# Kernel optimization log

Hardware: AMD Instinct MI355X
Metric: run time of the kernel (lower is better)

Reference implementation:

```python
import jax, jax.numpy as jnp
import numpy as np

H = 512; NH = 8; L = 2; NPRED = 26; MAXF = 5; FF = 4 * H


def _ln(x, w, b, eps=1e-5):
    m = x.mean(-1, keepdims=True)
    v = ((x - m) ** 2).mean(-1, keepdims=True)
    return (x - m) / jnp.sqrt(v + eps) * w + b


def _gelu(x):
    return jax.nn.gelu(x, approximate=False)


def _mha(q_in, kv_in, in_w, in_b, out_w, out_b, nh=NH):
    # PyTorch nn.MultiheadAttention math (batch_first), no mask, eval mode.
    h = q_in.shape[-1]; dh = h // nh
    Wq, Wk, Wv = in_w[:h], in_w[h:2 * h], in_w[2 * h:]
    bq, bk, bv = in_b[:h], in_b[h:2 * h], in_b[2 * h:]
    B, Tq, _ = q_in.shape
    Tk = kv_in.shape[1]
    q = (q_in @ Wq.T + bq).reshape(B, Tq, nh, dh)
    k = (kv_in @ Wk.T + bk).reshape(B, Tk, nh, dh)
    v = (kv_in @ Wv.T + bv).reshape(B, Tk, nh, dh)
    s = jnp.einsum('bqhd,bkhd->bhqk', q, k) / jnp.sqrt(jnp.asarray(dh, q.dtype))
    a = jax.nn.softmax(s, axis=-1)
    o = jnp.einsum('bhqk,bkhd->bqhd', a, v).reshape(B, Tq, h)
    return o @ out_w.T + out_b


def setup_inputs():
    key = jax.random.key(0)
    ks = iter(jax.random.split(key, 48))
    r = lambda *s: jax.random.normal(next(ks), s, jnp.float32) * 0.02
    inp = {
        'temporal_context': jax.random.normal(next(ks), (16, 10, H), jnp.float32),
        'object_features': jax.random.normal(next(ks), (16, 20, H), jnp.float32),
        'future_queries': r(MAXF, H),
        'sa_in_w': r(L, 3 * H, H), 'sa_in_b': jnp.zeros((L, 3 * H), jnp.float32),
        'sa_out_w': r(L, H, H), 'sa_out_b': jnp.zeros((L, H), jnp.float32),
        'ca_in_w': r(L, 3 * H, H), 'ca_in_b': jnp.zeros((L, 3 * H), jnp.float32),
        'ca_out_w': r(L, H, H), 'ca_out_b': jnp.zeros((L, H), jnp.float32),
        'ff1_w': r(L, FF, H), 'ff1_b': jnp.zeros((L, FF), jnp.float32),
        'ff2_w': r(L, H, FF), 'ff2_b': jnp.zeros((L, H), jnp.float32),
        'n1_w': jnp.ones((L, H), jnp.float32), 'n1_b': jnp.zeros((L, H), jnp.float32),
        'n2_w': jnp.ones((L, H), jnp.float32), 'n2_b': jnp.zeros((L, H), jnp.float32),
        'n3_w': jnp.ones((L, H), jnp.float32), 'n3_b': jnp.zeros((L, H), jnp.float32),
        'norm_w': jnp.ones((H,), jnp.float32), 'norm_b': jnp.zeros((H,), jnp.float32),
        'pe1_w': r(H, 3 * H), 'pe1_b': jnp.zeros((H,), jnp.float32),
        'pe2_w': r(H, H), 'pe2_b': jnp.zeros((H,), jnp.float32),
        'pred_w': r(NPRED, H), 'pred_b': jnp.zeros((NPRED,), jnp.float32),
        'ex_w': r(1, H), 'ex_b': jnp.zeros((1,), jnp.float32),
        'num_future_frames': 5,
    }
    return inp


def reference(temporal_context, object_features, future_queries, sa_in_w, sa_in_b,
              sa_out_w, sa_out_b, ca_in_w, ca_in_b, ca_out_w, ca_out_b,
              ff1_w, ff1_b, ff2_w, ff2_b, n1_w, n1_b, n2_w, n2_b, n3_w, n3_b,
              norm_w, norm_b, pe1_w, pe1_b, pe2_w, pe2_b, pred_w, pred_b,
              ex_w, ex_b, num_future_frames):
    B = temporal_context.shape[0]
    Fh = num_future_frames
    # Future queries expanded over batch -> TransformerDecoder (post-norm, gelu, eval)
    x = jnp.broadcast_to(future_queries[:Fh][None], (B, Fh, H))
    mem = temporal_context
    for l in range(L):
        x = _ln(x + _mha(x, x, sa_in_w[l], sa_in_b[l], sa_out_w[l], sa_out_b[l]), n1_w[l], n1_b[l])
        x = _ln(x + _mha(x, mem, ca_in_w[l], ca_in_b[l], ca_out_w[l], ca_out_b[l]), n2_w[l], n2_b[l])
        ff = _gelu(x @ ff1_w[l].T + ff1_b[l]) @ ff2_w[l].T + ff2_b[l]
        x = _ln(x + ff, n3_w[l], n3_b[l])
    ctx = _ln(x, norm_w, norm_b)  # (B, F, H)
    # Vectorized (i, j) pair construction, i != j, in the original loop order
    N = object_features.shape[1]
    ii, jj = np.nonzero(~np.eye(N, dtype=bool))  # row-major == for i: for j: skip i==j
    P = ii.shape[0]
    subj = object_features[:, ii]  # (B, P, H)
    obj = object_features[:, jj]   # (B, P, H)
    pair = jnp.concatenate([
        jnp.broadcast_to(subj[:, None], (B, Fh, P, H)),
        jnp.broadcast_to(obj[:, None], (B, Fh, P, H)),
        jnp.broadcast_to(ctx[:, :, None], (B, Fh, P, H)),
    ], axis=-1)  # (B, F, P, 3H)
    enc = _gelu(pair @ pe1_w.T + pe1_b) @ pe2_w.T + pe2_b  # (B, F, P, H)
    predicate_logits = enc @ pred_w.T + pred_b  # (B, F, P, 26)
    existence_logits = enc @ ex_w.T + ex_b      # (B, F, P, 1)
    return predicate_logits, existence_logits
```

## Files before the change

### kernel.cpp

```cpp
#include <hip/hip_runtime.h>
#include <math.h>

#define HD 512
#define FFD 2048
#define FH 5
#define TM 10
#define NO 20
#define NP 380
#define PRED_N 790400

#define XM_PLAIN 0
#define XM_GELU  1
#define XM_FQ    2
#define XM_LN    3
#define XM_LN2   4

typedef short bf16x8 __attribute__((ext_vector_type(8)));
typedef float floatx4 __attribute__((ext_vector_type(4)));

__device__ __forceinline__ float gelu_f(float v) {
    return 0.5f * v * (1.0f + erff(v * 0.70710678118654752440f));
}
__device__ __forceinline__ unsigned short f2bf(float x) {
    unsigned int u = __float_as_uint(x);
    u = (u + 0x7FFFu + ((u >> 16) & 1u)) >> 16;
    return (unsigned short)u;
}

__device__ __forceinline__ void gemm_body(
    int bx, int by, int bz,
    const float* __restrict__ X, int ldx, int xmode,
    const float* __restrict__ parts, int np, int pzstr,
    const float* __restrict__ bo,
    const float* __restrict__ lw, const float* __restrict__ lb,
    const float* __restrict__ fw, const float* __restrict__ fb,
    float* __restrict__ xout, int xmod, int gps,
    const float* __restrict__ W, int ldw,
    float* __restrict__ Y, int ldy, int zyoff,
    int Klen, float* lds)
{
    float* Wt = lds;
    float* Xs = lds + 8256;
    int t = threadIdx.x;
    int nb = bx * 128;
    int z  = bz;
    int rt = (xmode >= XM_LN) ? 8 : 16;
    int r0 = by * rt;
    int kbase = z * Klen;
    float* Yb = Y + (size_t)z * zyoff;
    int c  = t & 31;
    int rg = t >> 5;
    int sc = t >> 4;
    int q  = t & 15;

    if (xmode >= XM_LN) {
        int rl = t >> 5;
        int r  = r0 + rl;
        int c0 = (t & 31) * 16;
        int rr = xmod ? (r % xmod) : r;
        float v[16];
        #pragma unroll
        for (int u = 0; u < 16; u += 4) {
            float4 a = *(const float4*)(X + (size_t)rr * ldx + c0 + u);
            float4 bb = *(const float4*)(bo + c0 + u);
            float vx = a.x + bb.x, vy = a.y + bb.y, vz = a.z + bb.z, vw = a.w + bb.w;
            for (int zz = 0; zz < np; ++zz) {
                float4 p = *(const float4*)(parts + (size_t)zz * pzstr + (size_t)r * HD + c0 + u);
                vx += p.x; vy += p.y; vz += p.z; vw += p.w;
            }
            v[u] = vx; v[u + 1] = vy; v[u + 2] = vz; v[u + 3] = vw;
        }
        float s1 = 0, s2 = 0;
        #pragma unroll
        for (int u = 0; u < 16; ++u) { s1 += v[u]; s2 += v[u] * v[u]; }
        #pragma unroll
        for (int o = 16; o > 0; o >>= 1) {
            s1 += __shfl_down(s1, o, 32);
            s2 += __shfl_down(s2, o, 32);
        }
        s1 = __shfl(s1, 0, 32); s2 = __shfl(s2, 0, 32);
        float mean = s1 * (1.0f / HD);
        float rstd = rsqrtf(s2 * (1.0f / HD) - mean * mean + 1e-5f);
        #pragma unroll
        for (int u = 0; u < 16; ++u)
            v[u] = (v[u] - mean) * rstd * lw[c0 + u] + lb[c0 + u];
        if (xout && z == 0 && bx == 0) {
            #pragma unroll
            for (int u = 0; u < 16; u += 4)
                *(float4*)(xout + (size_t)r * HD + c0 + u) =
                    make_float4(v[u], v[u + 1], v[u + 2], v[u + 3]);
        }
        if (xmode == XM_LN2) {
            float t1 = 0, t2 = 0;
            #pragma unroll
            for (int u = 0; u < 16; ++u) { t1 += v[u]; t2 += v[u] * v[u]; }
            #pragma unroll
            for (int o = 16; o > 0; o >>= 1) {
                t1 += __shfl_down(t1, o, 32);
                t2 += __shfl_down(t2, o, 32);
            }
            t1 = __shfl(t1, 0, 32); t2 = __shfl(t2, 0, 32);
            float m2 = t1 * (1.0f / HD);
            float rs2 = rsqrtf(t2 * (1.0f / HD) - m2 * m2 + 1e-5f);
            #pragma unroll
            for (int u = 0; u < 16; ++u)
                v[u] = (v[u] - m2) * rs2 * fw[c0 + u] + fb[c0 + u];
        }
        #pragma unroll
        for (int u = 0; u < 16; u += 4)
            *(float4*)(Xs + rl * HD + c0 + u) =
                make_float4(v[u], v[u + 1], v[u + 2], v[u + 3]);
        __syncthreads();
    }

    float a00 = 0, a01 = 0, a02 = 0, a03 = 0;
    float a10 = 0, a11 = 0, a12 = 0, a13 = 0;

    for (int kc = 0; kc < Klen; kc += 64) {
        int kg = kbase + kc;
        if (xmode <= XM_FQ) {
            float4 xv;
            if (xmode == XM_PLAIN) {
                xv = *(const float4*)(X + (size_t)(r0 + sc) * ldx + kg + q * 4);
            } else if (xmode == XM_FQ) {
                xv = *(const float4*)(X + (size_t)((r0 + sc) % FH) * ldx + kg + q * 4);
            } else {
                const float* p0 = X + (size_t)(r0 + sc) * ldx + kg + q * 4;
                float4 a = *(const float4*)p0;
                float4 b = *(const float4*)(p0 + gps);
                float4 bi = *(const float4*)(bo + kg + q * 4);
                xv.x = gelu_f(a.x + b.x + bi.x);
                xv.y = gelu_f(a.y + b.y + bi.y);
                xv.z = gelu_f(a.z + b.z + bi.z);
                xv.w = gelu_f(a.w + b.w + bi.w);
            }
            *(float4*)&Xs[sc * 64 + q * 4] = xv;
        }
        #pragma unroll
        for (int p = 0; p < 8; ++p) {
            int cc = sc + p * 16;
            float4 wv = *(const float4*)(W + (size_t)(nb + cc) * ldw + kg + q * 4);
            Wt[(q * 4 + 0) * 129 + cc] = wv.x;
            Wt[(q * 4 + 1) * 129 + cc] = wv.y;
            Wt[(q * 4 + 2) * 129 + cc] = wv.z;
            Wt[(q * 4 + 3) * 129 + cc] = wv.w;
        }
        __syncthreads();
        if (rt == 16) {
            const float* xr0 = &Xs[(rg * 2 + 0) * 64];
            const float* xr1 = &Xs[(rg * 2 + 1) * 64];
            #pragma unroll
            for (int k4 = 0; k4 < 16; ++k4) {
                float4 x0 = *(const float4*)(xr0 + k4 * 4);
                float4 x1 = *(const float4*)(xr1 + k4 * 4);
                const float* x0p = (const float*)&x0;
                const float* x1p = (const float*)&x1;
                #pragma unroll
                for (int i = 0; i < 4; ++i) {
                    const float* wrow = &Wt[(k4 * 4 + i) * 129 + c];
                    float w0 = wrow[0], w1 = wrow[32], w2 = wrow[64], w3 = wrow[96];
                    float xi0 = x0p[i], xi1 = x1p[i];
                    a00 = fmaf(xi0, w0, a00); a01 = fmaf(xi0, w1, a01);
                    a02 = fmaf(xi0, w2, a02); a03 = fmaf(xi0, w3, a03);
                    a10 = fmaf(xi1, w0, a10); a11 = fmaf(xi1, w1, a11);
                    a12 = fmaf(xi1, w2, a12); a13 = fmaf(xi1, w3, a13);
                }
            }
        } else {
            const float* xr0 = &Xs[rg * HD + kg];
            #pragma unroll
            for (int k4 = 0; k4 < 16; ++k4) {
                float4 x0 = *(const float4*)(xr0 + k4 * 4);
                const float* x0p = (const float*)&x0;
                #pragma unroll
                for (int i = 0; i < 4; ++i) {
                    const float* wrow = &Wt[(k4 * 4 + i) * 129 + c];
                    float xi0 = x0p[i];
                    a00 = fmaf(xi0, wrow[0],  a00);
                    a01 = fmaf(xi0, wrow[32], a01);
                    a02 = fmaf(xi0, wrow[64], a02);
                    a03 = fmaf(xi0, wrow[96], a03);
                }
            }
        }
        __syncthreads();
    }
    if (rt == 16) {
        float* yr = Yb + (size_t)(r0 + rg * 2) * ldy + nb + c;
        yr[0] = a00; yr[32] = a01; yr[64] = a02; yr[96] = a03;
        yr += ldy;
        yr[0] = a10; yr[32] = a11; yr[64] = a12; yr[96] = a13;
    } else {
        float* yr = Yb + (size_t)(r0 + rg) * ldy + nb + c;
        yr[0] = a00; yr[32] = a01; yr[64] = a02; yr[96] = a03;
    }
}

__global__ __launch_bounds__(256) void k_gemm(
    const float* __restrict__ X, int ldx, int xmode,
    const float* __restrict__ parts, int np, int pzstr,
    const float* __restrict__ bo,
    const float* __restrict__ lw, const float* __restrict__ lb,
    const float* __restrict__ fw, const float* __restrict__ fb,
    float* __restrict__ xout, int xmod, int gps,
    const float* __restrict__ W, int ldw,
    float* __restrict__ Y, int ldy, int zyoff, int Klen)
{
    __shared__ float lds[12352];
    gemm_body(blockIdx.x, blockIdx.y, blockIdx.z, X, ldx, xmode, parts, np, pzstr,
              bo, lw, lb, fw, fb, xout, xmod, gps, W, ldw, Y, ldy, zyoff, Klen, lds);
}

__device__ void mprep(int m, const float* __restrict__ pe2_w, const float* __restrict__ pe2_b,
                      const float* __restrict__ pred_w, const float* __restrict__ pred_b,
                      const float* __restrict__ ex_w, const float* __restrict__ ex_b,
                      unsigned short* __restrict__ Mbf, float* __restrict__ cb, float* lds)
{
    int t = threadIdx.x;
    if (m < 16) {
        int dl = t & 31, ec = t >> 5;
        int d = m * 32 + dl;
        float acc[27];
        #pragma unroll
        for (int k = 0; k < 27; ++k) acc[k] = 0.f;
        for (int e = ec * 64; e < ec * 64 + 64; ++e) {
            float wv = pe2_w[(size_t)e * HD + d];
            #pragma unroll
            for (int k = 0; k < 26; ++k) acc[k] = fmaf(wv, pred_w[k * HD + e], acc[k]);
            acc[26] = fmaf(wv, ex_w[e], acc[26]);
        }
        #pragma unroll
        for (int k = 0; k < 27; ++k) lds[(ec * 32 + dl) * 27 + k] = acc[k];
        __syncthreads();
        for (int idx = t; idx < 1024; idx += 256) {
            int dl2 = idx >> 5, k = idx & 31;
            float s = 0.f;
            if (k < 27) {
                #pragma unroll
                for (int e = 0; e < 8; ++e) s += lds[(e * 32 + dl2) * 27 + k];
            }
            int quad = dl2 >> 3, j = dl2 & 7;
            int nt = k >> 4, n15 = k & 15;
            int lane = quad * 16 + n15;
            Mbf[((size_t)(m * 2 + nt) * 64 + lane) * 8 + j] = f2bf(s);
        }
    } else {
        int g = t >> 3, li = t & 7;
        if (g < 27) {
            const float* wo = (g < 26) ? (pred_w + g * HD) : ex_w;
            float a = 0.f;
            for (int e = li; e < HD; e += 8) a += pe2_b[e] * wo[e];
            a += __shfl_down(a, 4, 8);
            a += __shfl_down(a, 2, 8);
            a += __shfl_down(a, 1, 8);
            if (li == 0) cb[g] = a + ((g < 26) ? pred_b[g] : ex_b[0]);
        }
    }
}

__global__ __launch_bounds__(256) void k_prep(
    const float* __restrict__ objf, const float* __restrict__ temporal,
    const float* __restrict__ pe1_w, const float* __restrict__ ca_in_w,
    const float* __restrict__ pe2_w, const float* __restrict__ pe2_b,
    const float* __restrict__ pred_w, const float* __restrict__ pred_b,
    const float* __restrict__ ex_w, const float* __restrict__ ex_b,
    float* __restrict__ SOp, float* __restrict__ kvb,
    unsigned short* __restrict__ Mbf, float* __restrict__ cb)
{
    __shared__ float lds[12352];
    int blk = blockIdx.x;
    if (blk < 320) {
        int zw = blk & 1, zk = (blk >> 1) & 1, ct = (blk >> 2) & 3, y = blk >> 4;
        gemm_body(ct, y, zk, objf, HD, XM_PLAIN, nullptr, 0, 0,
                  nullptr, nullptr, nullptr, nullptr, nullptr, nullptr, 0, 0,
                  pe1_w + zw * 512, 1536,
                  SOp + zw * 512, 1024, 327680, 256, lds);
    } else if (blk < 640) {
        int s = blk - 320;
        int ct = s & 7, l = (s >> 3) & 1, zk = (s >> 4) & 1, y = s >> 5;
        gemm_body(ct, y, zk, temporal, HD, XM_PLAIN, nullptr, 0, 0,
                  nullptr, nullptr, nullptr, nullptr, nullptr, nullptr, 0, 0,
                  ca_in_w + (size_t)(l * 1536 + 512) * HD, HD,
                  kvb + (size_t)((zk * 2 + l) * 160) * 1024, 1024, 0, 256, lds);
    } else {
        mprep(blk - 640, pe2_w, pe2_b, pred_w, pred_b, ex_w, ex_b, Mbf, cb, lds);
    }
}

__global__ __launch_bounds__(256) void k_attnsa_proj(
    int l, const float* __restrict__ qkvp, const float* __restrict__ in_b,
    const float* __restrict__ Wout, float* __restrict__ yp)
{
    __shared__ float lds[11008];
    int bi = blockIdx.x;
    int b = bi >> 4, ct = (bi >> 2) & 3, zk = bi & 3;
    int t = threadIdx.x;
    float* qkv = lds;
    float* sc  = lds + 7680;
    float* aw  = lds + 7880;
    float* ao  = lds + 8448;
    float* Wt  = lds;

    for (int idx = t; idx < 1920; idx += 256) {
        int tok = idx / 384, c4 = (idx % 384) * 4;
        size_t o = (size_t)(b * FH + tok) * 1536 + c4;
        float4 v = *(const float4*)(in_b + l * 1536 + c4);
        #pragma unroll
        for (int z = 0; z < 4; ++z) {
            float4 p = *(const float4*)(qkvp + (size_t)z * 122880 + o);
            v.x += p.x; v.y += p.y; v.z += p.z; v.w += p.w;
        }
        int m = c4 >> 9, d = c4 & 511;
        *(float4*)(qkv + (size_t)(m * FH + tok) * 512 + d) = v;
    }
    __syncthreads();
    if (t < 200) {
        int h = t / 25, tq = (t / 5) % 5, tu = t % 5;
        float s = 0;
        for (int d = 0; d < 64; ++d)
            s += qkv[tq * 512 + h * 64 + d] * qkv[(FH + tu) * 512 + h * 64 + d];
        sc[t] = s * 0.125f;
    }
    __syncthreads();
    if (t < 40) {
        int base = (t / 5) * 25 + (t % 5) * 5;
        float mx = -1e30f;
        for (int u = 0; u < 5; ++u) mx = fmaxf(mx, sc[base + u]);
        float e[5], sm = 0;
        for (int u = 0; u < 5; ++u) { e[u] = expf(sc[base + u] - mx); sm += e[u]; }
        for (int u = 0; u < 5; ++u) aw[base + u] = e[u] / sm;
    }
    __syncthreads();
    for (int idx = t; idx < 2560; idx += 256) {
        int tok = idx >> 9, c = idx & 511, h = c >> 6;
        float s = 0;
        #pragma unroll
        for (int u = 0; u < 5; ++u)
            s += aw[h * 25 + tok * 5 + u] * qkv[(2 * FH + u) * 512 + c];
        ao[tok * 512 + c] = s;
    }
    int c = t & 31, rg = t >> 5;
    int nb = ct * 128;
    float a0 = 0, a1 = 0, a2 = 0, a3 = 0;
    for (int ch = 0; ch < 2; ++ch) {
        int kg = zk * 128 + ch * 64;
        __syncthreads();
        for (int idx = t; idx < 2048; idx += 256) {
            int cc = idx >> 4, qq = idx & 15;
            float4 wv = *(const float4*)(Wout + (size_t)(nb + cc) * HD + kg + qq * 4);
            Wt[(qq * 4 + 0) * 129 + cc] = wv.x;
            Wt[(qq * 4 + 1) * 129 + cc] = wv.y;
            Wt[(qq * 4 + 2) * 129 + cc] = wv.z;
            Wt[(qq * 4 + 3) * 129 + cc] = wv.w;
        }
        __syncthreads();
        if (rg < FH) {
            const float* xr = ao + rg * 512 + kg;
            #pragma unroll
            for (int k4 = 0; k4 < 16; ++k4) {
                float4 xv = *(const float4*)(xr + k4 * 4);
                #pragma unroll
                for (int i = 0; i < 4; ++i) {
                    const float* wr = &Wt[(k4 * 4 + i) * 129 + c];
                    float x = ((const float*)&xv)[i];
                    a0 = fmaf(x, wr[0],  a0); a1 = fmaf(x, wr[32], a1);
                    a2 = fmaf(x, wr[64], a2); a3 = fmaf(x, wr[96], a3);
                }
            }
        }
    }
    if (rg < FH) {
        float* yr = yp + (size_t)zk * 40960 + (size_t)(b * FH + rg) * HD + nb + c;
        yr[0] = a0; yr[32] = a1; yr[64] = a2; yr[96] = a3;
    }
}

__global__ __launch_bounds__(256) void k_attnca_proj(
    int l, const float* __restrict__ qp, const float* __restrict__ kvb,
    const float* __restrict__ in_b, const float* __restrict__ Wout,
    float* __restrict__ yp)
{
    __shared__ float lds[16160];
    int bi = blockIdx.x;
    int b = bi >> 4, ct = (bi >> 2) & 3, zk = bi & 3;
    int t = threadIdx.x;
    float* q  = lds;
    float* kl = lds + 2560;
    float* vl = lds + 7680;
    float* sc = lds + 12800;
    float* aw = lds + 13200;
    float* ao = lds + 13600;
    float* Wt = lds;
    const float* bb = in_b + l * 1536;

    for (int idx = t; idx < 640; idx += 256) {
        int tok = idx / 128, c4 = (idx % 128) * 4;
        size_t o = (size_t)(b * FH + tok) * HD + c4;
        float4 v = *(const float4*)(bb + c4);
        #pragma unroll
        for (int z = 0; z < 4; ++z) {
            float4 p = *(const float4*)(qp + (size_t)z * 40960 + o);
            v.x += p.x; v.y += p.y; v.z += p.z; v.w += p.w;
        }
        *(float4*)(q + tok * 512 + c4) = v;
    }
    for (int idx = t; idx < 1280; idx += 256) {
        int u = idx / 128, c4 = (idx % 128) * 4;
        size_t base = (size_t)(l * 160 + b * TM + u) * 1024;
        float4 k0 = *(const float4*)(kvb + base + c4);
        float4 k1 = *(const float4*)(kvb + 327680 + base + c4);
        float4 bk = *(const float4*)(bb + 512 + c4);
        float4 v0 = *(const float4*)(kvb + base + 512 + c4);
        float4 v1 = *(const float4*)(kvb + 327680 + base + 512 + c4);
        float4 bv = *(const float4*)(bb + 1024 + c4);
        *(float4*)(kl + u * 512 + c4) = make_float4(k0.x + k1.x + bk.x, k0.y + k1.y + bk.y,
                                                    k0.z + k1.z + bk.z, k0.w + k1.w + bk.w);
        *(float4*)(vl + u * 512 + c4) = make_float4(v0.x + v1.x + bv.x, v0.y + v1.y + bv.y,
                                                    v0.z + v1.z + bv.z, v0.w + v1.w + bv.w);
    }
    __syncthreads();
    for (int idx = t; idx < 400; idx += 256) {
        int h = idx / 50, tq = (idx / 10) % 5, tu = idx % 10;
        float s = 0;
        for (int d = 0; d < 64; ++d)
            s += q[tq * 512 + h * 64 + d] * kl[tu * 512 + h * 64 + d];
        sc[idx] = s * 0.125f;
    }
    __syncthreads();
    if (t < 40) {
        int base = (t / 5) * 50 + (t % 5) * 10;
        float mx = -1e30f;
        for (int u = 0; u < TM; ++u) mx = fmaxf(mx, sc[base + u]);
        float e[TM], sm = 0;
        for (int u = 0; u < TM; ++u) { e[u] = expf(sc[base + u] - mx); sm += e[u]; }
        for (int u = 0; u < TM; ++u) aw[base + u] = e[u] / sm;
    }
    __syncthreads();
    for (int idx = t; idx < 2560; idx += 256) {
        int tok = idx >> 9, c = idx & 511, h = c >> 6;
        float s = 0;
        #pragma unroll
        for (int u = 0; u < TM; ++u)
            s += aw[h * 50 + tok * 10 + u] * vl[u * 512 + c];
        ao[tok * 512 + c] = s;
    }
    int c = t & 31, rg = t >> 5;
    int nb = ct * 128;
    float a0 = 0, a1 = 0, a2 = 0, a3 = 0;
    for (int ch = 0; ch < 2; ++ch) {
        int kg = zk * 128 + ch * 64;
        __syncthreads();
        for (int idx = t; idx < 2048; idx += 256) {
            int cc = idx >> 4, qq = idx & 15;
            float4 wv = *(const float4*)(Wout + (size_t)(nb + cc) * HD + kg + qq * 4);
            Wt[(qq * 4 + 0) * 129 + cc] = wv.x;
            Wt[(qq * 4 + 1) * 129 + cc] = wv.y;
            Wt[(qq * 4 + 2) * 129 + cc] = wv.z;
            Wt[(qq * 4 + 3) * 129 + cc] = wv.w;
        }
        __syncthreads();
        if (rg < FH) {
            const float* xr = ao + rg * 512 + kg;
            #pragma unroll
            for (int k4 = 0; k4 < 16; ++k4) {
                float4 xv = *(const float4*)(xr + k4 * 4);
                #pragma unroll
                for (int i = 0; i < 4; ++i) {
                    const float* wr = &Wt[(k4 * 4 + i) * 129 + c];
                    float x = ((const float*)&xv)[i];
                    a0 = fmaf(x, wr[0],  a0); a1 = fmaf(x, wr[32], a1);
                    a2 = fmaf(x, wr[64], a2); a3 = fmaf(x, wr[96], a3);
                }
            }
        }
    }
    if (rg < FH) {
        float* yr = yp + (size_t)zk * 40960 + (size_t)(b * FH + rg) * HD + nb + c;
        yr[0] = a0; yr[32] = a1; yr[64] = a2; yr[96] = a3;
    }
}

__global__ __launch_bounds__(256) void k_pair(
    const float* __restrict__ SOp, const float* __restrict__ cpb,
    const float* __restrict__ pe1_b,
    const unsigned short* __restrict__ Mbf, const float* __restrict__ cb,
    float* __restrict__ out)
{
    __shared__ float lds[14964];
    int blk = blockIdx.x;
    int third = blk % 3, bf = blk / 3;
    int b = bf / FH, f = bf % FH;
    int t = threadIdx.x;
    int wv = t >> 6, lane = t & 63;
    int quad = lane >> 4, n15 = lane & 15;
    int i0 = (third == 0) ? 0 : (third == 1 ? 6 : 13);

    for (int idx = t; idx < 29 * 128; idx += 256) {
        int row = idx >> 7, c4 = (idx & 127) << 2;
        float4 v;
        if (row < 8) {
            int i = i0 + row; if (i > 19) i = 19;
            size_t o = (size_t)(b * NO + i) * 1024 + c4;
            float4 p0 = *(const float4*)(SOp + o);
            float4 p1 = *(const float4*)(SOp + 327680 + o);
            v = make_float4(p0.x + p1.x, p0.y + p1.y, p0.z + p1.z, p0.w + p1.w);
        } else if (row < 28) {
            int j = row - 8;
            size_t o = (size_t)(b * NO + j) * 1024 + 512 + c4;
            float4 p0 = *(const float4*)(SOp + o);
            float4 p1 = *(const float4*)(SOp + 327680 + o);
            v = make_float4(p0.x + p1.x, p0.y + p1.y, p0.z + p1.z, p0.w + p1.w);
        } else {
            size_t o = (size_t)(b * FH + f) * HD + c4;
            float4 s = *(const float4*)(cpb + o);
            #pragma unroll
            for (int z = 1; z < 4; ++z) {
                float4 p = *(const float4*)(cpb + (size_t)z * 40960 + o);
                s.x += p.x; s.y += p.y; s.z += p.z; s.w += p.w;
            }
            float4 pb = *(const float4*)(pe1_b + c4);
            v = make_float4(s.x + pb.x, s.y + pb.y, s.z + pb.z, s.w + pb.w);
        }
        *(float4*)(lds + row * 516 + c4) = v;
    }
    __syncthreads();

    floatx4 acc00 = {0,0,0,0}, acc01 = {0,0,0,0}, acc10 = {0,0,0,0}, acc11 = {0,0,0,0};
    for (int ks = 0; ks < 16; ++ks) {
        bf16x8 b0 = *(const bf16x8*)(Mbf + ((size_t)(ks * 2 + 0) * 64 + lane) * 8);
        bf16x8 b1 = *(const bf16x8*)(Mbf + ((size_t)(ks * 2 + 1) * 64 + lane) * 8);
        #pragma unroll
        for (int mt = 0; mt < 2; ++mt) {
            int p = third * 128 + wv * 32 + mt * 16 + n15;
            bf16x8 afr = {0, 0, 0, 0, 0, 0, 0, 0};
            if (p < NP) {
                int i = p / 19, j0 = p % 19;
                int j = j0 + (j0 >= i ? 1 : 0);
                int dof = ks * 32 + quad * 8;
                const float* Sr = lds + (i - i0) * 516 + dof;
                const float* Or = lds + (8 + j) * 516 + dof;
                const float* Cr = lds + 28 * 516 + dof;
                float4 sa = *(const float4*)Sr, sb = *(const float4*)(Sr + 4);
                float4 oa = *(const float4*)Or, ob = *(const float4*)(Or + 4);
                float4 ca = *(const float4*)Cr, cc = *(const float4*)(Cr + 4);
                union { unsigned short u[8]; bf16x8 v8; } pk;
                pk.u[0] = f2bf(gelu_f(sa.x + oa.x + ca.x));
                pk.u[1] = f2bf(gelu_f(sa.y + oa.y + ca.y));
                pk.u[2] = f2bf(gelu_f(sa.z + oa.z + ca.z));
                pk.u[3] = f2bf(gelu_f(sa.w + oa.w + ca.w));
                pk.u[4] = f2bf(gelu_f(sb.x + ob.x + cc.x));
                pk.u[5] = f2bf(gelu_f(sb.y + ob.y + cc.y));
                pk.u[6] = f2bf(gelu_f(sb.z + ob.z + cc.z));
                pk.u[7] = f2bf(gelu_f(sb.w + ob.w + cc.w));
                afr = pk.v8;
            }
            if (mt == 0) {
                acc00 = __builtin_amdgcn_mfma_f32_16x16x32_bf16(afr, b0, acc00, 0, 0, 0);
                acc01 = __builtin_amdgcn_mfma_f32_16x16x32_bf16(afr, b1, acc01, 0, 0, 0);
            } else {
                acc10 = __builtin_amdgcn_mfma_f32_16x16x32_bf16(afr, b0, acc10, 0, 0, 0);
                acc11 = __builtin_amdgcn_mfma_f32_16x16x32_bf16(afr, b1, acc11, 0, 0, 0);
            }
        }
    }
    int pbase = (b * FH + f) * NP;
    #pragma unroll
    for (int mt = 0; mt < 2; ++mt) {
        #pragma unroll
        for (int nt = 0; nt < 2; ++nt) {
            floatx4 a = (mt == 0) ? (nt == 0 ? acc00 : acc01)
                                  : (nt == 0 ? acc10 : acc11);
            int n = nt * 16 + n15;
            #pragma unroll
            for (int reg = 0; reg < 4; ++reg) {
                int p = third * 128 + wv * 32 + mt * 16 + quad * 4 + reg;
                if (p < NP && n < 27) {
                    float vout = a[reg] + cb[n];
                    if (n < 26) out[(size_t)(pbase + p) * 26 + n] = vout;
                    else        out[PRED_N + pbase + p] = vout;
                }
            }
        }
    }
}

extern "C" void kernel_launch(void* const* d_in, const int* in_sizes, int n_in,
                              void* d_out, int out_size, void* d_ws, size_t ws_size,
                              hipStream_t stream) {
    const float* temporal = (const float*)d_in[0];
    const float* objf     = (const float*)d_in[1];
    const float* fq       = (const float*)d_in[2];
    const float* sa_in_w  = (const float*)d_in[3];
    const float* sa_in_b  = (const float*)d_in[4];
    const float* sa_out_w = (const float*)d_in[5];
    const float* sa_out_b = (const float*)d_in[6];
    const float* ca_in_w  = (const float*)d_in[7];
    const float* ca_in_b  = (const float*)d_in[8];
    const float* ca_out_w = (const float*)d_in[9];
    const float* ca_out_b = (const float*)d_in[10];
    const float* ff1_w    = (const float*)d_in[11];
    const float* ff1_b    = (const float*)d_in[12];
    const float* ff2_w    = (const float*)d_in[13];
    const float* ff2_b    = (const float*)d_in[14];
    const float* n1_w     = (const float*)d_in[15];
    const float* n1_b     = (const float*)d_in[16];
    const float* n2_w     = (const float*)d_in[17];
    const float* n2_b     = (const float*)d_in[18];
    const float* n3_w     = (const float*)d_in[19];
    const float* n3_b     = (const float*)d_in[20];
    const float* norm_w   = (const float*)d_in[21];
    const float* norm_b   = (const float*)d_in[22];
    const float* pe1_w    = (const float*)d_in[23];
    const float* pe1_b    = (const float*)d_in[24];
    const float* pe2_w    = (const float*)d_in[25];
    const float* pe2_b    = (const float*)d_in[26];
    const float* pred_w   = (const float*)d_in[27];
    const float* pred_b   = (const float*)d_in[28];
    const float* ex_w     = (const float*)d_in[29];
    const float* ex_b     = (const float*)d_in[30];

    float* ws   = (float*)d_ws;
    float* x1   = ws;
    float* x2   = ws + 40960;
    float* x3   = ws + 81920;
    float* qkvp = ws + 122880;
    float* qp   = ws + 614400;
    float* yp   = ws + 778240;
    float* ffp  = ws + 1105920;
    float* kvb  = ws + 1433600;
    float* SOp  = ws + 2088960;
    float* cpb  = ws + 2744320;
    unsigned short* Mbf = (unsigned short*)(ws + 2908160);
    float* cb   = ws + 2916352;
    float* out  = (float*)d_out;

    k_prep<<<657, 256, 0, stream>>>(objf, temporal, pe1_w, ca_in_w,
                                    pe2_w, pe2_b, pred_w, pred_b, ex_w, ex_b,
                                    SOp, kvb, Mbf, cb);
    for (int l = 0; l < 2; ++l) {
        if (l == 0) {
            k_gemm<<<dim3(12, 5, 4), 256, 0, stream>>>(
                fq, HD, XM_FQ, nullptr, 0, 0, nullptr, nullptr, nullptr,
                nullptr, nullptr, nullptr, 0, 0,
                sa_in_w, HD, qkvp, 1536, 122880, 128);
        } else {
            k_gemm<<<dim3(12, 10, 4), 256, 0, stream>>>(
                x2, HD, XM_LN, yp, 8, 40960, ff2_b, n3_w, n3_b,
                nullptr, nullptr, x3, 0, 0,
                sa_in_w + 786432, HD, qkvp, 1536, 122880, 128);
        }
        k_attnsa_proj<<<256, 256, 0, stream>>>(l, qkvp, sa_in_b,
                                               sa_out_w + (size_t)l * 262144, yp);
        k_gemm<<<dim3(4, 10, 4), 256, 0, stream>>>(
            (l == 0 ? fq : x3), HD, XM_LN, yp, 4, 40960,
            sa_out_b + l * HD, n1_w + l * HD, n1_b + l * HD,
            nullptr, nullptr, x1, (l == 0 ? FH : 0), 0,
            ca_in_w + (size_t)l * 786432, HD, qp, HD, 40960, 128);
        k_attnca_proj<<<256, 256, 0, stream>>>(l, qp, kvb, ca_in_b,
                                               ca_out_w + (size_t)l * 262144, yp);
        k_gemm<<<dim3(16, 10, 2), 256, 0, stream>>>(
            x1, HD, XM_LN, yp, 4, 40960,
            ca_out_b + l * HD, n2_w + l * HD, n2_b + l * HD,
            nullptr, nullptr, x2, 0, 0,
            ff1_w + (size_t)l * 1048576, HD, ffp, FFD, 163840, 256);
        k_gemm<<<dim3(4, 5, 8), 256, 0, stream>>>(
            ffp, FFD, XM_GELU, nullptr, 0, 0, ff1_b + l * FFD,
            nullptr, nullptr, nullptr, nullptr, nullptr, 0, 163840,
            ff2_w + (size_t)l * 1048576, FFD, yp, HD, 40960, 256);
    }
    k_gemm<<<dim3(4, 10, 4), 256, 0, stream>>>(
        x2, HD, XM_LN2, yp, 8, 40960, ff2_b + HD, n3_w + HD, n3_b + HD,
        norm_w, norm_b, nullptr, 0, 0,
        pe1_w + 1024, 1536, cpb, HD, 40960, 128);
    k_pair<<<240, 256, 0, stream>>>(SOp, cpb, pe1_b, Mbf, cb, out);
}
```

Measured before the change: 415.5 us.

## Register-prefetch next K-chunk in GEMMs, template xmode, and slice attention by column

The GEMM body becomes a template on the input mode, so mode branches resolve at compile time and each mode gets its own LDS size. It prefetches the next 64-wide chunk of weights and inputs into registers while computing the current one, which also drops one barrier per iteration. The attention+projection kernels now load only the 128-column slice that each block's split-K projection needs, rather than the full 512 columns of Q/K/V. This cuts redundant global loads and LDS use, and the first weight chunk is prefetched before attention starts. The cost is higher register pressure from the prefetch buffers.

Result: faster. 381.0 us (-8.3%).

```diff
diff --git a/kernel.cpp b/kernel.cpp
--- a/kernel.cpp
+++ b/kernel.cpp
@@ -27,9 +27,10 @@
     return (unsigned short)u;
 }
 
+template <int XMODE>
 __device__ __forceinline__ void gemm_body(
     int bx, int by, int bz,
-    const float* __restrict__ X, int ldx, int xmode,
+    const float* __restrict__ X, int ldx,
     const float* __restrict__ parts, int np, int pzstr,
     const float* __restrict__ bo,
     const float* __restrict__ lw, const float* __restrict__ lb,
@@ -41,19 +42,15 @@
 {
     float* Wt = lds;
     float* Xs = lds + 8256;
+    const int RT = (XMODE >= XM_LN) ? 8 : 16;
     int t = threadIdx.x;
     int nb = bx * 128;
-    int z  = bz;
-    int rt = (xmode >= XM_LN) ? 8 : 16;
-    int r0 = by * rt;
-    int kbase = z * Klen;
-    float* Yb = Y + (size_t)z * zyoff;
-    int c  = t & 31;
-    int rg = t >> 5;
-    int sc = t >> 4;
-    int q  = t & 15;
-
-    if (xmode >= XM_LN) {
+    int r0 = by * RT;
+    int kbase = bz * Klen;
+    float* Yb = Y + (size_t)bz * zyoff;
+    int c = t & 31, rg = t >> 5, scs = t >> 4, q = t & 15;
+
+    if (XMODE >= XM_LN) {
         int rl = t >> 5;
         int r  = r0 + rl;
         int c0 = (t & 31) * 16;
@@ -84,13 +81,13 @@
         #pragma unroll
         for (int u = 0; u < 16; ++u)
             v[u] = (v[u] - mean) * rstd * lw[c0 + u] + lb[c0 + u];
-        if (xout && z == 0 && bx == 0) {
+        if (xout && bz == 0 && bx == 0) {
             #pragma unroll
             for (int u = 0; u < 16; u += 4)
                 *(float4*)(xout + (size_t)r * HD + c0 + u) =
                     make_float4(v[u], v[u + 1], v[u + 2], v[u + 3]);
         }
-        if (xmode == XM_LN2) {
+        if (XMODE == XM_LN2) {
             float t1 = 0, t2 = 0;
             #pragma unroll
             for (int u = 0; u < 16; ++u) { t1 += v[u]; t2 += v[u] * v[u]; }
@@ -116,37 +113,66 @@
     float a00 = 0, a01 = 0, a02 = 0, a03 = 0;
     float a10 = 0, a11 = 0, a12 = 0, a13 = 0;
 
-    for (int kc = 0; kc < Klen; kc += 64) {
-        int kg = kbase + kc;
-        if (xmode <= XM_FQ) {
+    int nch = Klen >> 6;
+    float4 wreg[8];
+    float4 xra, xrb, xrc;
+    {
+        int kg = kbase;
+        #pragma unroll
+        for (int p = 0; p < 8; ++p)
+            wreg[p] = *(const float4*)(W + (size_t)(nb + scs + p * 16) * ldw + kg + q * 4);
+        if (XMODE == XM_PLAIN) {
+            xra = *(const float4*)(X + (size_t)(r0 + scs) * ldx + kg + q * 4);
+        } else if (XMODE == XM_FQ) {
+            xra = *(const float4*)(X + (size_t)((r0 + scs) % FH) * ldx + kg + q * 4);
+        } else if (XMODE == XM_GELU) {
+            const float* p0 = X + (size_t)(r0 + scs) * ldx + kg + q * 4;
+            xra = *(const float4*)p0;
+            xrb = *(const float4*)(p0 + gps);
+            xrc = *(const float4*)(bo + kg + q * 4);
+        }
+    }
+
+    for (int ch = 0; ch < nch; ++ch) {
+        if (ch) __syncthreads();
+        if (XMODE <= XM_FQ) {
             float4 xv;
-            if (xmode == XM_PLAIN) {
-                xv = *(const float4*)(X + (size_t)(r0 + sc) * ldx + kg + q * 4);
-            } else if (xmode == XM_FQ) {
-                xv = *(const float4*)(X + (size_t)((r0 + sc) % FH) * ldx + kg + q * 4);
+            if (XMODE == XM_GELU) {
+                xv.x = gelu_f(xra.x + xrb.x + xrc.x);
+                xv.y = gelu_f(xra.y + xrb.y + xrc.y);
+                xv.z = gelu_f(xra.z + xrb.z + xrc.z);
+                xv.w = gelu_f(xra.w + xrb.w + xrc.w);
             } else {
-                const float* p0 = X + (size_t)(r0 + sc) * ldx + kg + q * 4;
-                float4 a = *(const float4*)p0;
-                float4 b = *(const float4*)(p0 + gps);
-                float4 bi = *(const float4*)(bo + kg + q * 4);
-                xv.x = gelu_f(a.x + b.x + bi.x);
-                xv.y = gelu_f(a.y + b.y + bi.y);
-                xv.z = gelu_f(a.z + b.z + bi.z);
-                xv.w = gelu_f(a.w + b.w + bi.w);
-            }
-            *(float4*)&Xs[sc * 64 + q * 4] = xv;
+                xv = xra;
+            }
+            *(float4*)&Xs[scs * 64 + q * 4] = xv;
         }
         #pragma unroll
         for (int p = 0; p < 8; ++p) {
-            int cc = sc + p * 16;
-            float4 wv = *(const float4*)(W + (size_t)(nb + cc) * ldw + kg + q * 4);
-            Wt[(q * 4 + 0) * 129 + cc] = wv.x;
-            Wt[(q * 4 + 1) * 129 + cc] = wv.y;
-            Wt[(q * 4 + 2) * 129 + cc] = wv.z;
-            Wt[(q * 4 + 3) * 129 + cc] = wv.w;
+            int cc = scs + p * 16;
+            Wt[(q * 4 + 0) * 129 + cc] = wreg[p].x;
+            Wt[(q * 4 + 1) * 129 + cc] = wreg[p].y;
+            Wt[(q * 4 + 2) * 129 + cc] = wreg[p].z;
+            Wt[(q * 4 + 3) * 129 + cc] = wreg[p].w;
         }
         __syncthreads();
-        if (rt == 16) {
+        if (ch + 1 < nch) {
+            int kg = kbase + (ch + 1) * 64;
+            #pragma unroll
+            for (int p = 0; p < 8; ++p)
+                wreg[p] = *(const float4*)(W + (size_t)(nb + scs + p * 16) * ldw + kg + q * 4);
+            if (XMODE == XM_PLAIN) {
+                xra = *(const float4*)(X + (size_t)(r0 + scs) * ldx + kg + q * 4);
+            } else if (XMODE == XM_FQ) {
+                xra = *(const float4*)(X + (size_t)((r0 + scs) % FH) * ldx + kg + q * 4);
+            } else if (XMODE == XM_GELU) {
+                const float* p0 = X + (size_t)(r0 + scs) * ldx + kg + q * 4;
+                xra = *(const float4*)p0;
+                xrb = *(const float4*)(p0 + gps);
+                xrc = *(const float4*)(bo + kg + q * 4);
+            }
+        }
+        if (RT == 16) {
             const float* xr0 = &Xs[(rg * 2 + 0) * 64];
             const float* xr1 = &Xs[(rg * 2 + 1) * 64];
             #pragma unroll
@@ -167,7 +193,7 @@
                 }
             }
         } else {
-            const float* xr0 = &Xs[rg * HD + kg];
+            const float* xr0 = &Xs[rg * HD + kbase + ch * 64];
             #pragma unroll
             for (int k4 = 0; k4 < 16; ++k4) {
                 float4 x0 = *(const float4*)(xr0 + k4 * 4);
@@ -183,9 +209,8 @@
                 }
             }
         }
-        __syncthreads();
-    }
-    if (rt == 16) {
+    }
+    if (RT == 16) {
         float* yr = Yb + (size_t)(r0 + rg * 2) * ldy + nb + c;
         yr[0] = a00; yr[32] = a01; yr[64] = a02; yr[96] = a03;
         yr += ldy;
@@ -196,8 +221,9 @@
     }
 }
 
+template <int XMODE>
 __global__ __launch_bounds__(256) void k_gemm(
-    const float* __restrict__ X, int ldx, int xmode,
+    const float* __restrict__ X, int ldx,
     const float* __restrict__ parts, int np, int pzstr,
     const float* __restrict__ bo,
     const float* __restrict__ lw, const float* __restrict__ lb,
@@ -206,9 +232,10 @@
     const float* __restrict__ W, int ldw,
     float* __restrict__ Y, int ldy, int zyoff, int Klen)
 {
-    __shared__ float lds[12352];
-    gemm_body(blockIdx.x, blockIdx.y, blockIdx.z, X, ldx, xmode, parts, np, pzstr,
-              bo, lw, lb, fw, fb, xout, xmod, gps, W, ldw, Y, ldy, zyoff, Klen, lds);
+    __shared__ float lds[(XMODE >= XM_LN) ? 12352 : 9280];
+    gemm_body<XMODE>(blockIdx.x, blockIdx.y, blockIdx.z, X, ldx, parts, np, pzstr,
+                     bo, lw, lb, fw, fb, xout, xmod, gps, W, ldw, Y, ldy, zyoff,
+                     Klen, lds);
 }
 
 __device__ void mprep(int m, const float* __restrict__ pe2_w, const float* __restrict__ pe2_b,
@@ -267,21 +294,23 @@
     float* __restrict__ SOp, float* __restrict__ kvb,
     unsigned short* __restrict__ Mbf, float* __restrict__ cb)
 {
-    __shared__ float lds[12352];
+    __shared__ float lds[9280];
     int blk = blockIdx.x;
     if (blk < 320) {
         int zw = blk & 1, zk = (blk >> 1) & 1, ct = (blk >> 2) & 3, y = blk >> 4;
-        gemm_body(ct, y, zk, objf, HD, XM_PLAIN, nullptr, 0, 0,
-                  nullptr, nullptr, nullptr, nullptr, nullptr, nullptr, 0, 0,
-                  pe1_w + zw * 512, 1536,
-                  SOp + zw * 512, 1024, 327680, 256, lds);
+        gemm_body<XM_PLAIN>(ct, y, zk, objf, HD, nullptr, 0, 0,
+                            nullptr, nullptr, nullptr, nullptr, nullptr,
+                            nullptr, 0, 0,
+                            pe1_w + zw * 512, 1536,
+                            SOp + zw * 512, 1024, 327680, 256, lds);
     } else if (blk < 640) {
         int s = blk - 320;
         int ct = s & 7, l = (s >> 3) & 1, zk = (s >> 4) & 1, y = s >> 5;
-        gemm_body(ct, y, zk, temporal, HD, XM_PLAIN, nullptr, 0, 0,
-                  nullptr, nullptr, nullptr, nullptr, nullptr, nullptr, 0, 0,
-                  ca_in_w + (size_t)(l * 1536 + 512) * HD, HD,
-                  kvb + (size_t)((zk * 2 + l) * 160) * 1024, 1024, 0, 256, lds);
+        gemm_body<XM_PLAIN>(ct, y, zk, temporal, HD, nullptr, 0, 0,
+                            nullptr, nullptr, nullptr, nullptr, nullptr,
+                            nullptr, 0, 0,
+                            ca_in_w + (size_t)(l * 1536 + 512) * HD, HD,
+                            kvb + (size_t)((zk * 2 + l) * 160) * 1024, 1024, 0, 256, lds);
     } else {
         mprep(blk - 640, pe2_w, pe2_b, pred_w, pred_b, ex_w, ex_b, Mbf, cb, lds);
     }
@@ -291,38 +320,47 @@
     int l, const float* __restrict__ qkvp, const float* __restrict__ in_b,
     const float* __restrict__ Wout, float* __restrict__ yp)
 {
-    __shared__ float lds[11008];
+    __shared__ float lds[8896];
     int bi = blockIdx.x;
     int b = bi >> 4, ct = (bi >> 2) & 3, zk = bi & 3;
     int t = threadIdx.x;
     float* qkv = lds;
-    float* sc  = lds + 7680;
-    float* aw  = lds + 7880;
-    float* ao  = lds + 8448;
+    float* sc  = lds + 1920;
+    float* aw  = lds + 1984;
+    float* ao  = lds + 8256;
     float* Wt  = lds;
-
-    for (int idx = t; idx < 1920; idx += 256) {
-        int tok = idx / 384, c4 = (idx % 384) * 4;
-        size_t o = (size_t)(b * FH + tok) * 1536 + c4;
-        float4 v = *(const float4*)(in_b + l * 1536 + c4);
+    int col0 = zk * 128;
+    int c = t & 31, rg = t >> 5, scs = t >> 4, q = t & 15;
+    int nb = ct * 128;
+
+    float4 wreg[8];
+    #pragma unroll
+    for (int p = 0; p < 8; ++p)
+        wreg[p] = *(const float4*)(Wout + (size_t)(nb + scs + p * 16) * HD + col0 + q * 4);
+
+    for (int idx = t; idx < 480; idx += 256) {
+        int m = idx / 160, r = idx - m * 160;
+        int tok = r >> 5, c4 = (r & 31) * 4;
+        int col = m * HD + col0 + c4;
+        size_t o = (size_t)(b * FH + tok) * 1536 + col;
+        float4 v = *(const float4*)(in_b + l * 1536 + col);
         #pragma unroll
         for (int z = 0; z < 4; ++z) {
             float4 p = *(const float4*)(qkvp + (size_t)z * 122880 + o);
             v.x += p.x; v.y += p.y; v.z += p.z; v.w += p.w;
         }
-        int m = c4 >> 9, d = c4 & 511;
-        *(float4*)(qkv + (size_t)(m * FH + tok) * 512 + d) = v;
-    }
-    __syncthreads();
-    if (t < 200) {
-        int h = t / 25, tq = (t / 5) % 5, tu = t % 5;
+        *(float4*)(qkv + (m * FH + tok) * 128 + c4) = v;
+    }
+    __syncthreads();
+    if (t < 50) {
+        int hh = t / 25, r = t - hh * 25, tq = r / 5, tu = r % 5;
         float s = 0;
         for (int d = 0; d < 64; ++d)
-            s += qkv[tq * 512 + h * 64 + d] * qkv[(FH + tu) * 512 + h * 64 + d];
+            s += qkv[tq * 128 + hh * 64 + d] * qkv[(FH + tu) * 128 + hh * 64 + d];
         sc[t] = s * 0.125f;
     }
     __syncthreads();
-    if (t < 40) {
+    if (t < 10) {
         int base = (t / 5) * 25 + (t % 5) * 5;
         float mx = -1e30f;
         for (int u = 0; u < 5; ++u) mx = fmaxf(mx, sc[base + u]);
@@ -331,31 +369,35 @@
         for (int u = 0; u < 5; ++u) aw[base + u] = e[u] / sm;
     }
     __syncthreads();
-    for (int idx = t; idx < 2560; idx += 256) {
-        int tok = idx >> 9, c = idx & 511, h = c >> 6;
+    for (int idx = t; idx < 640; idx += 256) {
+        int tok = idx >> 7, cc = idx & 127, hh = cc >> 6;
         float s = 0;
         #pragma unroll
         for (int u = 0; u < 5; ++u)
-            s += aw[h * 25 + tok * 5 + u] * qkv[(2 * FH + u) * 512 + c];
-        ao[tok * 512 + c] = s;
-    }
-    int c = t & 31, rg = t >> 5;
-    int nb = ct * 128;
+            s += aw[hh * 25 + tok * 5 + u] * qkv[(2 * FH + u) * 128 + cc];
+        ao[tok * 128 + cc] = s;
+    }
+    __syncthreads();
+
     float a0 = 0, a1 = 0, a2 = 0, a3 = 0;
     for (int ch = 0; ch < 2; ++ch) {
-        int kg = zk * 128 + ch * 64;
+        if (ch) __syncthreads();
+        #pragma unroll
+        for (int p = 0; p < 8; ++p) {
+            int cc = scs + p * 16;
+            Wt[(q * 4 + 0) * 129 + cc] = wreg[p].x;
+            Wt[(q * 4 + 1) * 129 + cc] = wreg[p].y;
+            Wt[(q * 4 + 2) * 129 + cc] = wreg[p].z;
+            Wt[(q * 4 + 3) * 129 + cc] = wreg[p].w;
+        }
         __syncthreads();
-        for (int idx = t; idx < 2048; idx += 256) {
-            int cc = idx >> 4, qq = idx & 15;
-            float4 wv = *(const float4*)(Wout + (size_t)(nb + cc) * HD + kg + qq * 4);
-            Wt[(qq * 4 + 0) * 129 + cc] = wv.x;
-            Wt[(qq * 4 + 1) * 129 + cc] = wv.y;
-            Wt[(qq * 4 + 2) * 129 + cc] = wv.z;
-            Wt[(qq * 4 + 3) * 129 + cc] = wv.w;
-        }
-        __syncthreads();
+        if (ch == 0) {
+            #pragma unroll
+            for (int p = 0; p < 8; ++p)
+                wreg[p] = *(const float4*)(Wout + (size_t)(nb + scs + p * 16) * HD + col0 + 64 + q * 4);
+        }
         if (rg < FH) {
-            const float* xr = ao + rg * 512 + kg;
+            const float* xr = ao + rg * 128 + ch * 64;
             #pragma unroll
             for (int k4 = 0; k4 < 16; ++k4) {
                 float4 xv = *(const float4*)(xr + k4 * 4);
@@ -380,54 +422,64 @@
     const float* __restrict__ in_b, const float* __restrict__ Wout,
     float* __restrict__ yp)
 {
-    __shared__ float lds[16160];
+    __shared__ float lds[8896];
     int bi = blockIdx.x;
     int b = bi >> 4, ct = (bi >> 2) & 3, zk = bi & 3;
     int t = threadIdx.x;
-    float* q  = lds;
-    float* kl = lds + 2560;
-    float* vl = lds + 7680;
-    float* sc = lds + 12800;
-    float* aw = lds + 13200;
-    float* ao = lds + 13600;
+    float* qs = lds;
+    float* kl = lds + 640;
+    float* vl = lds + 1920;
+    float* sc = lds + 3200;
+    float* aw = lds + 3328;
+    float* ao = lds + 8256;
     float* Wt = lds;
     const float* bb = in_b + l * 1536;
-
-    for (int idx = t; idx < 640; idx += 256) {
-        int tok = idx / 128, c4 = (idx % 128) * 4;
-        size_t o = (size_t)(b * FH + tok) * HD + c4;
-        float4 v = *(const float4*)(bb + c4);
+    int col0 = zk * 128;
+    int c = t & 31, rg = t >> 5, scs = t >> 4, q = t & 15;
+    int nb = ct * 128;
+
+    float4 wreg[8];
+    #pragma unroll
+    for (int p = 0; p < 8; ++p)
+        wreg[p] = *(const float4*)(Wout + (size_t)(nb + scs + p * 16) * HD + col0 + q * 4);
+
+    if (t < 160) {
+        int tok = t >> 5, c4 = (t & 31) * 4;
+        size_t o = (size_t)(b * FH + tok) * HD + col0 + c4;
+        float4 v = *(const float4*)(bb + col0 + c4);
         #pragma unroll
         for (int z = 0; z < 4; ++z) {
             float4 p = *(const float4*)(qp + (size_t)z * 40960 + o);
             v.x += p.x; v.y += p.y; v.z += p.z; v.w += p.w;
         }
-        *(float4*)(q + tok * 512 + c4) = v;
-    }
-    for (int idx = t; idx < 1280; idx += 256) {
-        int u = idx / 128, c4 = (idx % 128) * 4;
+        *(float4*)(qs + tok * 128 + c4) = v;
+    }
+    for (int idx = t; idx < 320; idx += 256) {
+        int u = idx >> 5, c4 = (idx & 31) * 4;
         size_t base = (size_t)(l * 160 + b * TM + u) * 1024;
-        float4 k0 = *(const float4*)(kvb + base + c4);
-        float4 k1 = *(const float4*)(kvb + 327680 + base + c4);
-        float4 bk = *(const float4*)(bb + 512 + c4);
-        float4 v0 = *(const float4*)(kvb + base + 512 + c4);
-        float4 v1 = *(const float4*)(kvb + 327680 + base + 512 + c4);
-        float4 bv = *(const float4*)(bb + 1024 + c4);
-        *(float4*)(kl + u * 512 + c4) = make_float4(k0.x + k1.x + bk.x, k0.y + k1.y + bk.y,
-                                                    k0.z + k1.z + bk.z, k0.w + k1.w + bk.w);
-        *(float4*)(vl + u * 512 + c4) = make_float4(v0.x + v1.x + bv.x, v0.y + v1.y + bv.y,
-                                                    v0.z + v1.z + bv.z, v0.w + v1.w + bv.w);
-    }
-    __syncthreads();
-    for (int idx = t; idx < 400; idx += 256) {
-        int h = idx / 50, tq = (idx / 10) % 5, tu = idx % 10;
+        float4 k0 = *(const float4*)(kvb + base + col0 + c4);
+        float4 k1 = *(const float4*)(kvb + 327680 + base + col0 + c4);
+        float4 bk = *(const float4*)(bb + 512 + col0 + c4);
+        *(float4*)(kl + u * 128 + c4) =
+            make_float4(k0.x + k1.x + bk.x, k0.y + k1.y + bk.y,
+                        k0.z + k1.z + bk.z, k0.w + k1.w + bk.w);
+        float4 v0 = *(const float4*)(kvb + base + 512 + col0 + c4);
+        float4 v1 = *(const float4*)(kvb + 327680 + base + 512 + col0 + c4);
+        float4 bv = *(const float4*)(bb + 1024 + col0 + c4);
+        *(float4*)(vl + u * 128 + c4) =
+            make_float4(v0.x + v1.x + bv.x, v0.y + v1.y + bv.y,
+                        v0.z + v1.z + bv.z, v0.w + v1.w + bv.w);
+    }
+    __syncthreads();
+    if (t < 100) {
+        int hh = t / 50, r = t - hh * 50, tq = r / 10, tu = r % 10;
         float s = 0;
         for (int d = 0; d < 64; ++d)
-            s += q[tq * 512 + h * 64 + d] * kl[tu * 512 + h * 64 + d];
-        sc[idx] = s * 0.125f;
-    }
-    __syncthreads();
-    if (t < 40) {
+            s += qs[tq * 128 + hh * 64 + d] * kl[tu * 128 + hh * 64 + d];
+        sc[t] = s * 0.125f;
+    }
+    __syncthreads();
+    if (t < 10) {
         int base = (t / 5) * 50 + (t % 5) * 10;
         float mx = -1e30f;
         for (int u = 0; u < TM; ++u) mx = fmaxf(mx, sc[base + u]);
@@ -436,31 +488,35 @@
         for (int u = 0; u < TM; ++u) aw[base + u] = e[u] / sm;
     }
     __syncthreads();
-    for (int idx = t; idx < 2560; idx += 256) {
-        int tok = idx >> 9, c = idx & 511, h = c >> 6;
+    for (int idx = t; idx < 640; idx += 256) {
+        int tok = idx >> 7, cc = idx & 127, hh = cc >> 6;
         float s = 0;
         #pragma unroll
         for (int u = 0; u < TM; ++u)
-            s += aw[h * 50 + tok * 10 + u] * vl[u * 512 + c];
-        ao[tok * 512 + c] = s;
-    }
-    int c = t & 31, rg = t >> 5;
-    int nb = ct * 128;
+            s += aw[hh * 50 + tok * 10 + u] * vl[u * 128 + cc];
+        ao[tok * 128 + cc] = s;
+    }
+    __syncthreads();
+
     float a0 = 0, a1 = 0, a2 = 0, a3 = 0;
     for (int ch = 0; ch < 2; ++ch) {
-        int kg = zk * 128 + ch * 64;
+        if (ch) __syncthreads();
+        #pragma unroll
+        for (int p = 0; p < 8; ++p) {
+            int cc = scs + p * 16;
+            Wt[(q * 4 + 0) * 129 + cc] = wreg[p].x;
+            Wt[(q * 4 + 1) * 129 + cc] = wreg[p].y;
+            Wt[(q * 4 + 2) * 129 + cc] = wreg[p].z;
+            Wt[(q * 4 + 3) * 129 + cc] = wreg[p].w;
+        }
         __syncthreads();
-        for (int idx = t; idx < 2048; idx += 256) {
-            int cc = idx >> 4, qq = idx & 15;
-            float4 wv = *(const float4*)(Wout + (size_t)(nb + cc) * HD + kg + qq * 4);
-            Wt[(qq * 4 + 0) * 129 + cc] = wv.x;
-            Wt[(qq * 4 + 1) * 129 + cc] = wv.y;
-            Wt[(qq * 4 + 2) * 129 + cc] = wv.z;
-            Wt[(qq * 4 + 3) * 129 + cc] = wv.w;
-        }
-        __syncthreads();
+        if (ch == 0) {
+            #pragma unroll
+            for (int p = 0; p < 8; ++p)
+                wreg[p] = *(const float4*)(Wout + (size_t)(nb + scs + p * 16) * HD + col0 + 64 + q * 4);
+        }
         if (rg < FH) {
-            const float* xr = ao + rg * 512 + kg;
+            const float* xr = ao + rg * 128 + ch * 64;
             #pragma unroll
             for (int k4 = 0; k4 < 16; ++k4) {
                 float4 xv = *(const float4*)(xr + k4 * 4);
@@ -639,37 +695,37 @@
                                     SOp, kvb, Mbf, cb);
     for (int l = 0; l < 2; ++l) {
         if (l == 0) {
-            k_gemm<<<dim3(12, 5, 4), 256, 0, stream>>>(
-                fq, HD, XM_FQ, nullptr, 0, 0, nullptr, nullptr, nullptr,
+            k_gemm<XM_FQ><<<dim3(12, 5, 4), 256, 0, stream>>>(
+                fq, HD, nullptr, 0, 0, nullptr, nullptr, nullptr,
                 nullptr, nullptr, nullptr, 0, 0,
                 sa_in_w, HD, qkvp, 1536, 122880, 128);
         } else {
-            k_gemm<<<dim3(12, 10, 4), 256, 0, stream>>>(
-                x2, HD, XM_LN, yp, 8, 40960, ff2_b, n3_w, n3_b,
+            k_gemm<XM_LN><<<dim3(12, 10, 4), 256, 0, stream>>>(
+                x2, HD, yp, 8, 40960, ff2_b, n3_w, n3_b,
                 nullptr, nullptr, x3, 0, 0,
                 sa_in_w + 786432, HD, qkvp, 1536, 122880, 128);
         }
         k_attnsa_proj<<<256, 256, 0, stream>>>(l, qkvp, sa_in_b,
                                                sa_out_w + (size_t)l * 262144, yp);
-        k_gemm<<<dim3(4, 10, 4), 256, 0, stream>>>(
-            (l == 0 ? fq : x3), HD, XM_LN, yp, 4, 40960,
+        k_gemm<XM_LN><<<dim3(4, 10, 4), 256, 0, stream>>>(
+            (l == 0 ? fq : x3), HD, yp, 4, 40960,
             sa_out_b + l * HD, n1_w + l * HD, n1_b + l * HD,
             nullptr, nullptr, x1, (l == 0 ? FH : 0), 0,
             ca_in_w + (size_t)l * 786432, HD, qp, HD, 40960, 128);
         k_attnca_proj<<<256, 256, 0, stream>>>(l, qp, kvb, ca_in_b,
                                                ca_out_w + (size_t)l * 262144, yp);
-        k_gemm<<<dim3(16, 10, 2), 256, 0, stream>>>(
-            x1, HD, XM_LN, yp, 4, 40960,
+        k_gemm<XM_LN><<<dim3(16, 10, 2), 256, 0, stream>>>(
+            x1, HD, yp, 4, 40960,
             ca_out_b + l * HD, n2_w + l * HD, n2_b + l * HD,
             nullptr, nullptr, x2, 0, 0,
             ff1_w + (size_t)l * 1048576, HD, ffp, FFD, 163840, 256);
-        k_gemm<<<dim3(4, 5, 8), 256, 0, stream>>>(
-            ffp, FFD, XM_GELU, nullptr, 0, 0, ff1_b + l * FFD,
+        k_gemm<XM_GELU><<<dim3(4, 5, 8), 256, 0, stream>>>(
+            ffp, FFD, nullptr, 0, 0, ff1_b + l * FFD,
             nullptr, nullptr, nullptr, nullptr, nullptr, 0, 163840,
             ff2_w + (size_t)l * 1048576, FFD, yp, HD, 40960, 256);
     }
-    k_gemm<<<dim3(4, 10, 4), 256, 0, stream>>>(
-        x2, HD, XM_LN2, yp, 8, 40960, ff2_b + HD, n3_w + HD, n3_b + HD,
+    k_gemm<XM_LN2><<<dim3(4, 10, 4), 256, 0, stream>>>(
+        x2, HD, yp, 8, 40960, ff2_b + HD, n3_w + HD, n3_b + HD,
         norm_w, norm_b, nullptr, 0, 0,
         pe1_w + 1024, 1536, cpb, HD, 40960, 128);
     k_pair<<<240, 256, 0, stream>>>(SOp, cpb, pe1_b, Mbf, cb, out);
```
